# Kernel tuning notes

Hardware: AMD Instinct MI355X
Metric: run time of the kernel (lower is better)

The kernel has to match this reference:

```python
import jax, jax.numpy as jnp
import numpy as np

N = 50000
EH = 500000
ES = 250000
D_IN = 128
D_HID = 128
N_CLS = 47


def _mean_agg(feat, src, dst, n):
    # gather src features, scatter-mean onto dst (DGL copy_u + mean)
    msg = feat[src]                                   # [E, d]
    s = jax.ops.segment_sum(msg, dst, num_segments=n)  # [N, d]
    cnt = jax.ops.segment_sum(jnp.ones((src.shape[0],), feat.dtype), dst, num_segments=n)
    return s / jnp.maximum(cnt, 1.0)[:, None]


def _sage_cv_layer(H, HBar, W, b, hs, hd, ss, sd):
    hbar_new = _mean_agg(HBar, hs, hd, N)             # history etype
    hdelta_new = _mean_agg(H - HBar, ss, sd, N)       # sampled etype
    h_neigh = hbar_new + hdelta_new
    z = jnp.concatenate([H, h_neigh], axis=1)         # [N, 2*d_in]
    return jax.nn.relu(z @ W.T + b)


def setup_inputs() -> dict:
    key = jax.random.key(0)
    ks = jax.random.split(key, 16)
    gain = float(np.sqrt(2.0))  # calculate_gain('relu')

    def xavier(k, shape):
        fan_out, fan_in = shape
        a = gain * np.sqrt(6.0 / (fan_in + fan_out))
        return jax.random.uniform(k, shape, jnp.float32, -a, a)

    return {
        "x": jax.random.normal(ks[0], (N, D_IN), jnp.float32),
        "hbar0": jax.random.normal(ks[1], (N, D_IN), jnp.float32),
        "hbar1": jax.random.normal(ks[2], (N, D_HID), jnp.float32),
        "W0": xavier(ks[3], (D_HID, 2 * D_IN)),
        "b0": jnp.zeros((D_HID,), jnp.float32),
        "W1": xavier(ks[4], (N_CLS, 2 * D_HID)),
        "b1": jnp.zeros((N_CLS,), jnp.float32),
        "hist_src0": jax.random.randint(ks[5], (EH,), 0, N),
        "hist_dst0": jax.random.randint(ks[6], (EH,), 0, N),
        "samp_src0": jax.random.randint(ks[7], (ES,), 0, N),
        "samp_dst0": jax.random.randint(ks[8], (ES,), 0, N),
        "hist_src1": jax.random.randint(ks[9], (EH,), 0, N),
        "hist_dst1": jax.random.randint(ks[10], (EH,), 0, N),
        "samp_src1": jax.random.randint(ks[11], (ES,), 0, N),
        "samp_dst1": jax.random.randint(ks[12], (ES,), 0, N),
    }


def reference(x, hbar0, hbar1, W0, b0, W1, b1,
              hist_src0, hist_dst0, samp_src0, samp_dst0,
              hist_src1, hist_dst1, samp_src1, samp_dst1):
    h = _sage_cv_layer(x, hbar0, W0, b0, hist_src0, hist_dst0, samp_src0, samp_dst0)
    h = _sage_cv_layer(h, hbar1, W1, b1, hist_src1, hist_dst1, samp_src1, samp_dst1)
    return h  # [N, n_classes]
```

## Files before the change

kernel.cpp:

```cpp
#include <hip/hip_runtime.h>

#define D_FEAT 128
#define K_DIM  256
#define EPB 4096

typedef __attribute__((ext_vector_type(8))) short bf16x8;
typedef __attribute__((ext_vector_type(4))) float f32x4;

__device__ __forceinline__ unsigned short f2b(float f) {
    union { float f; unsigned u; } cv; cv.f = f;
    return (unsigned short)((cv.u + 0x7fffu + ((cv.u >> 16) & 1u)) >> 16);
}

__device__ __forceinline__ void addu4(float* a, uint4 v) {
    union { unsigned u; float f; } c;
    c.u = v.x << 16;         a[0] += c.f;
    c.u = v.x & 0xffff0000u; a[1] += c.f;
    c.u = v.y << 16;         a[2] += c.f;
    c.u = v.y & 0xffff0000u; a[3] += c.f;
    c.u = v.z << 16;         a[4] += c.f;
    c.u = v.z & 0xffff0000u; a[5] += c.f;
    c.u = v.w << 16;         a[6] += c.f;
    c.u = v.w & 0xffff0000u; a[7] += c.f;
}

__device__ __forceinline__ long yoff(int y, int EH, int ES) {
    return (long)((y + 1) >> 1) * EH + (long)(y >> 1) * ES;
}


__global__ __launch_bounds__(256)
void histB(const int* __restrict__ hd0, const int* __restrict__ sd0,
           const int* __restrict__ hd1, const int* __restrict__ sd1,
           int EH, int ES, int* __restrict__ bucketCnt, int nb2) {
    int y = blockIdx.y;
    const int* d = (y == 0) ? hd0 : (y == 1) ? sd0 : (y == 2) ? hd1 : sd1;
    int E = (y & 1) ? ES : EH;
    __shared__ int cnt[256];
    int t = threadIdx.x;
    cnt[t] = 0;
    __syncthreads();
    int i0 = blockIdx.x * EPB;
    #pragma unroll
    for (int j = 0; j < 16; ++j) {
        int i = i0 + j * 256 + t;
        if (i < E) atomicAdd(&cnt[d[i] >> 8], 1);
    }
    __syncthreads();
    if (t < nb2 && cnt[t] > 0) atomicAdd(&bucketCnt[y * nb2 + t], cnt[t]);
}

__global__ __launch_bounds__(64)
void scanBuckets(const int* __restrict__ bucketCnt, int* __restrict__ rpBucket,
                 int* __restrict__ bcur, int nb2) {
    int t = threadIdx.x;
    if (t < 4) {
        int run = 0;
        for (int i = 0; i < nb2; ++i) {
            rpBucket[t * (nb2 + 1) + i] = run;
            bcur[t * nb2 + i] = run;
            run += bucketCnt[t * nb2 + i];
        }
        rpBucket[t * (nb2 + 1) + nb2] = run;
    }
}

__global__ __launch_bounds__(256)
void binA(const int* __restrict__ hs0, const int* __restrict__ hd0,
          const int* __restrict__ ss0, const int* __restrict__ sd0,
          const int* __restrict__ hs1, const int* __restrict__ hd1,
          const int* __restrict__ ss1, const int* __restrict__ sd1,
          int EH, int ES, int* __restrict__ bcur, unsigned* __restrict__ recs,
          int nb2) {
    int y = blockIdx.y;
    const int* src = (y == 0) ? hs0 : (y == 1) ? ss0 : (y == 2) ? hs1 : ss1;
    const int* dst = (y == 0) ? hd0 : (y == 1) ? sd0 : (y == 2) ? hd1 : sd1;
    int E = (y & 1) ? ES : EH;
    unsigned* rb = recs + yoff(y, EH, ES);

    __shared__ int cnt[256];
    int t = threadIdx.x;
    cnt[t] = 0;
    __syncthreads();
    int i0 = blockIdx.x * EPB;
    #pragma unroll
    for (int j = 0; j < 16; ++j) {
        int i = i0 + j * 256 + t;
        if (i < E) atomicAdd(&cnt[dst[i] >> 8], 1);
    }
    __syncthreads();
    int c = cnt[t];
    __syncthreads();
    if (t < nb2 && c > 0) cnt[t] = atomicAdd(&bcur[y * nb2 + t], c);
    __syncthreads();
    #pragma unroll
    for (int j = 0; j < 16; ++j) {
        int i = i0 + j * 256 + t;
        if (i < E) {
            int dd = dst[i];
            int slot = atomicAdd(&cnt[dd >> 8], 1);
            rb[slot] = (unsigned)src[i] | ((unsigned)(dd & 255) << 24);
        }
    }
}

__global__ __launch_bounds__(256)
void placeB(const unsigned* __restrict__ recs, const int* __restrict__ rpBucket,
            int* __restrict__ rpAll, int* __restrict__ srcAll,
            int EH, int ES, int n, int nb2) {
    int y = blockIdx.y;
    int b = blockIdx.x;
    int E = (y & 1) ? ES : EH;
    int* rp = rpAll + (size_t)y * (n + 1);
    long off = yoff(y, EH, ES);
    const unsigned* rb = recs + off;
    int* sb = srcAll + off;
    int e0 = rpBucket[y * (nb2 + 1) + b];
    int e1 = rpBucket[y * (nb2 + 1) + b + 1];
    int nodeBase = b << 8;

    __shared__ int cnt[256];
    __shared__ int sh[256];
    int t = threadIdx.x;
    cnt[t] = 0;
    __syncthreads();
    for (int e = e0 + t; e < e1; e += 256)
        atomicAdd(&cnt[rb[e] >> 24], 1);
    __syncthreads();
    sh[t] = cnt[t];
    __syncthreads();
    for (int o = 1; o < 256; o <<= 1) {
        int x = (t >= o) ? sh[t - o] : 0;
        __syncthreads();
        sh[t] += x;
        __syncthreads();
    }
    int base = e0 + (t ? sh[t - 1] : 0);
    if (nodeBase + t < n) rp[nodeBase + t] = base;
    if (b == 0 && t == 0) rp[n] = E;
    cnt[t] = base;
    __syncthreads();
    for (int e = e0 + t; e < e1; e += 256) {
        unsigned r = rb[e];
        int p = atomicAdd(&cnt[r >> 24], 1);
        sb[p] = (int)(r & 0x00FFFFFFu);
    }
}

__global__ __launch_bounds__(256)
void prep_tables(const float4* __restrict__ H, const float4* __restrict__ HBar,
                 ushort4* __restrict__ hb, ushort4* __restrict__ db, int nvec) {
    int i = blockIdx.x * 256 + threadIdx.x;
    if (i >= nvec) return;
    float4 h = H[i], b = HBar[i];
    hb[i] = make_ushort4(f2b(b.x), f2b(b.y), f2b(b.z), f2b(b.w));
    db[i] = make_ushort4(f2b(h.x - b.x), f2b(h.y - b.y), f2b(h.z - b.z), f2b(h.w - b.w));
}

__global__ __launch_bounds__(256)
void conv_weights(const float* __restrict__ W0, unsigned short* __restrict__ Wb0,
                  const float* __restrict__ W1, unsigned short* __restrict__ Wb1) {
    int i = blockIdx.x * 256 + threadIdx.x;
    if (i < 128 * 256) Wb0[i] = f2b(W0[i]);
    if (i < 64 * 256) {
        int r = i >> 8;
        Wb1[i] = (r < 47) ? f2b(W1[i]) : (unsigned short)0;
    }
}

__global__ __launch_bounds__(256)
void aggregate_z(const float* __restrict__ H, const uint4* __restrict__ HB,
                 const uint4* __restrict__ DB,
                 const int* __restrict__ rpH, const int* __restrict__ srcH,
                 const int* __restrict__ rpS, const int* __restrict__ srcS,
                 uint4* __restrict__ z, int n) {
    int g    = blockIdx.x * 16 + (threadIdx.x >> 4);
    int lane = threadIdx.x & 15;
    if (g >= n) return;

    int hb_ = rpH[g], he = rpH[g + 1];
    int sb  = rpS[g], se = rpS[g + 1];

    float a[8] = {0, 0, 0, 0, 0, 0, 0, 0};
    int e = hb_;
    for (; e + 4 <= he; e += 4) {
        int s0 = srcH[e], s1 = srcH[e + 1], s2 = srcH[e + 2], s3 = srcH[e + 3];
        uint4 v0 = HB[(size_t)s0 * 16 + lane];
        uint4 v1 = HB[(size_t)s1 * 16 + lane];
        uint4 v2 = HB[(size_t)s2 * 16 + lane];
        uint4 v3 = HB[(size_t)s3 * 16 + lane];
        addu4(a, v0); addu4(a, v1); addu4(a, v2); addu4(a, v3);
    }
    for (; e < he; ++e) addu4(a, HB[(size_t)srcH[e] * 16 + lane]);

    float d[8] = {0, 0, 0, 0, 0, 0, 0, 0};
    e = sb;
    for (; e + 4 <= se; e += 4) {
        int s0 = srcS[e], s1 = srcS[e + 1], s2 = srcS[e + 2], s3 = srcS[e + 3];
        uint4 v0 = DB[(size_t)s0 * 16 + lane];
        uint4 v1 = DB[(size_t)s1 * 16 + lane];
        uint4 v2 = DB[(size_t)s2 * 16 + lane];
        uint4 v3 = DB[(size_t)s3 * 16 + lane];
        addu4(d, v0); addu4(d, v1); addu4(d, v2); addu4(d, v3);
    }
    for (; e < se; ++e) addu4(d, DB[(size_t)srcS[e] * 16 + lane]);

    float rH = 1.0f / fmaxf((float)(he - hb_), 1.0f);
    float rS = 1.0f / fmaxf((float)(se - sb), 1.0f);

    float nb0 = a[0] * rH + d[0] * rS, nb1 = a[1] * rH + d[1] * rS;
    float nb2 = a[2] * rH + d[2] * rS, nb3 = a[3] * rH + d[3] * rS;
    float nb4 = a[4] * rH + d[4] * rS, nb5 = a[5] * rH + d[5] * rS;
    float nb6 = a[6] * rH + d[6] * rS, nb7 = a[7] * rH + d[7] * rS;
    uint4 rv;
    rv.x = (unsigned)f2b(nb0) | ((unsigned)f2b(nb1) << 16);
    rv.y = (unsigned)f2b(nb2) | ((unsigned)f2b(nb3) << 16);
    rv.z = (unsigned)f2b(nb4) | ((unsigned)f2b(nb5) << 16);
    rv.w = (unsigned)f2b(nb6) | ((unsigned)f2b(nb7) << 16);
    z[(size_t)g * 32 + 16 + lane] = rv;

    const float4* H4 = (const float4*)H;
    float4 l0 = H4[(size_t)g * 32 + lane * 2];
    float4 l1 = H4[(size_t)g * 32 + lane * 2 + 1];
    uint4 lv;
    lv.x = (unsigned)f2b(l0.x) | ((unsigned)f2b(l0.y) << 16);
    lv.y = (unsigned)f2b(l0.z) | ((unsigned)f2b(l0.w) << 16);
    lv.z = (unsigned)f2b(l1.x) | ((unsigned)f2b(l1.y) << 16);
    lv.w = (unsigned)f2b(l1.z) | ((unsigned)f2b(l1.w) << 16);
    z[(size_t)g * 32 + lane] = lv;
}

template<int NT>
__global__ __launch_bounds__(256)
void gemm_mfma(const unsigned short* __restrict__ Z, const unsigned short* __restrict__ Wb,
               const float* __restrict__ bias, float* __restrict__ out, int n, int COLS) {
    int wave = threadIdx.x >> 6;
    int lane = threadIdx.x & 63;
    int m0 = blockIdx.x * 64 + wave * 16;
    int mr = m0 + (lane & 15);
    int mc = (mr < n) ? mr : (n - 1);
    int kq = lane >> 4;

    f32x4 acc[NT] = {};
    const short* Zs = (const short*)Z;
    const short* Ws = (const short*)Wb;

    #pragma unroll
    for (int k0 = 0; k0 < 8; ++k0) {
        int ko = k0 * 32 + kq * 8;
        bf16x8 aF = *(const bf16x8*)(Zs + (size_t)mc * 256 + ko);
        #pragma unroll
        for (int t = 0; t < NT; ++t) {
            bf16x8 bF = *(const bf16x8*)(Ws + (size_t)(t * 16 + (lane & 15)) * 256 + ko);
            acc[t] = __builtin_amdgcn_mfma_f32_16x16x32_bf16(aF, bF, acc[t], 0, 0, 0);
        }
    }

    int cl = lane & 15;
    int rg = (lane >> 4) * 4;
    #pragma unroll
    for (int t = 0; t < NT; ++t) {
        int c = t * 16 + cl;
        if (c >= COLS) continue;
        float bv = bias[c];
        #pragma unroll
        for (int r = 0; r < 4; ++r) {
            int m = m0 + rg + r;
            if (m < n) out[(size_t)m * COLS + c] = fmaxf(acc[t][r] + bv, 0.f);
        }
    }
}

extern "C" void kernel_launch(void* const* d_in, const int* in_sizes, int n_in,
                              void* d_out, int out_size, void* d_ws, size_t ws_size,
                              hipStream_t stream) {
    const float* x     = (const float*)d_in[0];
    const float* hbar0 = (const float*)d_in[1];
    const float* hbar1 = (const float*)d_in[2];
    const float* W0    = (const float*)d_in[3];
    const float* b0    = (const float*)d_in[4];
    const float* W1    = (const float*)d_in[5];
    const float* b1    = (const float*)d_in[6];
    const int* hs0 = (const int*)d_in[7];
    const int* hd0 = (const int*)d_in[8];
    const int* ss0 = (const int*)d_in[9];
    const int* sd0 = (const int*)d_in[10];
    const int* hs1 = (const int*)d_in[11];
    const int* hd1 = (const int*)d_in[12];
    const int* ss1 = (const int*)d_in[13];
    const int* sd1 = (const int*)d_in[14];

    const int n   = in_sizes[0] / D_FEAT;
    const int EH  = in_sizes[7];
    const int ES  = in_sizes[9];
    const int nb2 = (n + 255) / 256;

    int* bucketCnt = (int*)d_ws;
    int* rpBucket  = bucketCnt + 4 * nb2;
    int* bcur      = rpBucket + 4 * (nb2 + 1);
    int* rpAll     = bcur + 4 * nb2;
    int* srcAll    = rpAll + 4 * (size_t)(n + 1);
    size_t int_words = (size_t)12 * nb2 + 4 + 4 * (size_t)(n + 1)
                     + 2 * (size_t)EH + 2 * (size_t)ES;
    int_words = (int_words + 3) & ~(size_t)3;
    float* h1 = (float*)d_ws + int_words;
    unsigned short* hb  = (unsigned short*)(h1 + (size_t)n * D_FEAT);
    unsigned short* db  = hb + (size_t)n * D_FEAT;
    unsigned short* z   = db + (size_t)n * D_FEAT;
    unsigned short* Wb0 = z + (size_t)n * K_DIM;
    unsigned short* Wb1 = Wb0 + 128 * 256;
    unsigned* recs = (unsigned*)z;

    const int* rpH0 = rpAll;
    const int* rpS0 = rpAll + (size_t)(n + 1);
    const int* rpH1 = rpAll + 2 * (size_t)(n + 1);
    const int* rpS1 = rpAll + 3 * (size_t)(n + 1);
    int* srcH0 = srcAll;
    int* srcS0 = srcAll + (size_t)EH;
    int* srcH1 = srcAll + (size_t)EH + ES;
    int* srcS1 = srcAll + 2 * (size_t)EH + ES;

    dim3 blk(256);
    int binb  = (EH + EPB - 1) / EPB;
    int prepb = ((n * 32) + 255) / 256;
    int aggb  = (n + 15) / 16;
    int gemmb = (n + 63) / 64;

    hipMemsetAsync(bucketCnt, 0, 4 * (size_t)nb2 * sizeof(int), stream);
    conv_weights<<<128, blk, 0, stream>>>(W0, Wb0, W1, Wb1);
    histB<<<dim3(binb, 4), blk, 0, stream>>>(hd0, sd0, hd1, sd1, EH, ES, bucketCnt, nb2);
    scanBuckets<<<1, 64, 0, stream>>>(bucketCnt, rpBucket, bcur, nb2);
    binA<<<dim3(binb, 4), blk, 0, stream>>>(hs0, hd0, ss0, sd0, hs1, hd1, ss1, sd1,
                                            EH, ES, bcur, recs, nb2);
    placeB<<<dim3(nb2, 4), blk, 0, stream>>>(recs, rpBucket, rpAll, srcAll, EH, ES, n, nb2);

    prep_tables<<<prepb, blk, 0, stream>>>((const float4*)x, (const float4*)hbar0,
                                           (ushort4*)hb, (ushort4*)db, n * 32);
    aggregate_z<<<aggb, blk, 0, stream>>>(x, (const uint4*)hb, (const uint4*)db,
                                          rpH0, srcH0, rpS0, srcS0, (uint4*)z, n);
    gemm_mfma<8><<<gemmb, blk, 0, stream>>>(z, Wb0, b0, h1, n, 128);

    prep_tables<<<prepb, blk, 0, stream>>>((const float4*)h1, (const float4*)hbar1,
                                           (ushort4*)hb, (ushort4*)db, n * 32);
    aggregate_z<<<aggb, blk, 0, stream>>>(h1, (const uint4*)hb, (const uint4*)db,
                                          rpH1, srcH1, rpS1, srcS1, (uint4*)z, n);
    gemm_mfma<3><<<gemmb, blk, 0, stream>>>(z, Wb1, b1, (float*)d_out, n, 47);
}
```

Measured before the change: 353.2 us.

## Fuse layer-1 table prep into layer-0 GEMM epilogue and widen aggregation

Builds the bf16 tables for both layers in one static prep kernel: hbar0, x−hbar0, hbar1 and the self half of z from x. The layer-0 GEMM epilogue now writes relu output directly as bf16 into z's self half and as (h−hbar1) into the layer-1 delta table. This removes the fp32 h1 buffer, the second prep pass and the self-feature conversion in aggregation. Aggregation now uses a full 64-lane wave per node with eight edges in flight, followed by a shuffle reduction. The cost is more scattered 2-byte stores in the GEMM epilogue, an in-place read/write of z, and a larger workspace because the edge records move out of z.

```diff
diff --git a/kernel.cpp b/kernel.cpp
--- a/kernel.cpp
+++ b/kernel.cpp
@@ -10,6 +10,14 @@
 __device__ __forceinline__ unsigned short f2b(float f) {
     union { float f; unsigned u; } cv; cv.f = f;
     return (unsigned short)((cv.u + 0x7fffu + ((cv.u >> 16) & 1u)) >> 16);
+}
+
+__device__ __forceinline__ unsigned pack2(float lo, float hi) {
+    return (unsigned)f2b(lo) | ((unsigned)f2b(hi) << 16);
+}
+
+__device__ __forceinline__ uint4 pack8(float4 a, float4 b) {
+    return make_uint4(pack2(a.x, a.y), pack2(a.z, a.w), pack2(b.x, b.y), pack2(b.z, b.w));
 }
 
 __device__ __forceinline__ void addu4(float* a, uint4 v) {
@@ -148,13 +156,21 @@
 }
 
 __global__ __launch_bounds__(256)
-void prep_tables(const float4* __restrict__ H, const float4* __restrict__ HBar,
-                 ushort4* __restrict__ hb, ushort4* __restrict__ db, int nvec) {
+void prep_static(const float4* __restrict__ x, const float4* __restrict__ hbar0,
+                 const float4* __restrict__ hbar1,
+                 uint4* __restrict__ hb0, uint4* __restrict__ db0,
+                 uint4* __restrict__ hb1, uint4* __restrict__ z, int n16) {
     int i = blockIdx.x * 256 + threadIdx.x;
-    if (i >= nvec) return;
-    float4 h = H[i], b = HBar[i];
-    hb[i] = make_ushort4(f2b(b.x), f2b(b.y), f2b(b.z), f2b(b.w));
-    db[i] = make_ushort4(f2b(h.x - b.x), f2b(h.y - b.y), f2b(h.z - b.z), f2b(h.w - b.w));
+    if (i >= n16) return;
+    float4 xa = x[i * 2],     xb = x[i * 2 + 1];
+    float4 ba = hbar0[i * 2], bb = hbar0[i * 2 + 1];
+    float4 ca = hbar1[i * 2], cb = hbar1[i * 2 + 1];
+    hb0[i] = pack8(ba, bb);
+    db0[i] = pack8(make_float4(xa.x - ba.x, xa.y - ba.y, xa.z - ba.z, xa.w - ba.w),
+                   make_float4(xb.x - bb.x, xb.y - bb.y, xb.z - bb.z, xb.w - bb.w));
+    hb1[i] = pack8(ca, cb);
+    int g = i >> 4, seg = i & 15;
+    z[(size_t)g * 32 + seg] = pack8(xa, xb);
 }
 
 __global__ __launch_bounds__(256)
@@ -169,65 +185,93 @@
 }
 
 __global__ __launch_bounds__(256)
-void aggregate_z(const float* __restrict__ H, const uint4* __restrict__ HB,
-                 const uint4* __restrict__ DB,
+void aggregate_z(const uint4* __restrict__ HB, const uint4* __restrict__ DB,
                  const int* __restrict__ rpH, const int* __restrict__ srcH,
                  const int* __restrict__ rpS, const int* __restrict__ srcS,
                  uint4* __restrict__ z, int n) {
-    int g    = blockIdx.x * 16 + (threadIdx.x >> 4);
-    int lane = threadIdx.x & 15;
+    int g = blockIdx.x * 4 + (threadIdx.x >> 6);
     if (g >= n) return;
+    int lane = threadIdx.x & 63;
+    int j = lane >> 4, l = lane & 15;
 
     int hb_ = rpH[g], he = rpH[g + 1];
     int sb  = rpS[g], se = rpS[g + 1];
 
     float a[8] = {0, 0, 0, 0, 0, 0, 0, 0};
-    int e = hb_;
-    for (; e + 4 <= he; e += 4) {
-        int s0 = srcH[e], s1 = srcH[e + 1], s2 = srcH[e + 2], s3 = srcH[e + 3];
-        uint4 v0 = HB[(size_t)s0 * 16 + lane];
-        uint4 v1 = HB[(size_t)s1 * 16 + lane];
-        uint4 v2 = HB[(size_t)s2 * 16 + lane];
-        uint4 v3 = HB[(size_t)s3 * 16 + lane];
-        addu4(a, v0); addu4(a, v1); addu4(a, v2); addu4(a, v3);
-    }
-    for (; e < he; ++e) addu4(a, HB[(size_t)srcH[e] * 16 + lane]);
-
+    for (int e0 = hb_; e0 < he; e0 += 8) {
+        int e1 = e0 + j, e2 = e0 + 4 + j;
+        uint4 v1 = make_uint4(0, 0, 0, 0), v2 = make_uint4(0, 0, 0, 0);
+        if (e1 < he) v1 = HB[(size_t)srcH[e1] * 16 + l];
+        if (e2 < he) v2 = HB[(size_t)srcH[e2] * 16 + l];
+        addu4(a, v1); addu4(a, v2);
+    }
     float d[8] = {0, 0, 0, 0, 0, 0, 0, 0};
-    e = sb;
-    for (; e + 4 <= se; e += 4) {
-        int s0 = srcS[e], s1 = srcS[e + 1], s2 = srcS[e + 2], s3 = srcS[e + 3];
-        uint4 v0 = DB[(size_t)s0 * 16 + lane];
-        uint4 v1 = DB[(size_t)s1 * 16 + lane];
-        uint4 v2 = DB[(size_t)s2 * 16 + lane];
-        uint4 v3 = DB[(size_t)s3 * 16 + lane];
-        addu4(d, v0); addu4(d, v1); addu4(d, v2); addu4(d, v3);
-    }
-    for (; e < se; ++e) addu4(d, DB[(size_t)srcS[e] * 16 + lane]);
+    for (int e0 = sb; e0 < se; e0 += 8) {
+        int e1 = e0 + j, e2 = e0 + 4 + j;
+        uint4 v1 = make_uint4(0, 0, 0, 0), v2 = make_uint4(0, 0, 0, 0);
+        if (e1 < se) v1 = DB[(size_t)srcS[e1] * 16 + l];
+        if (e2 < se) v2 = DB[(size_t)srcS[e2] * 16 + l];
+        addu4(d, v1); addu4(d, v2);
+    }
 
     float rH = 1.0f / fmaxf((float)(he - hb_), 1.0f);
     float rS = 1.0f / fmaxf((float)(se - sb), 1.0f);
-
-    float nb0 = a[0] * rH + d[0] * rS, nb1 = a[1] * rH + d[1] * rS;
-    float nb2 = a[2] * rH + d[2] * rS, nb3 = a[3] * rH + d[3] * rS;
-    float nb4 = a[4] * rH + d[4] * rS, nb5 = a[5] * rH + d[5] * rS;
-    float nb6 = a[6] * rH + d[6] * rS, nb7 = a[7] * rH + d[7] * rS;
-    uint4 rv;
-    rv.x = (unsigned)f2b(nb0) | ((unsigned)f2b(nb1) << 16);
-    rv.y = (unsigned)f2b(nb2) | ((unsigned)f2b(nb3) << 16);
-    rv.z = (unsigned)f2b(nb4) | ((unsigned)f2b(nb5) << 16);
-    rv.w = (unsigned)f2b(nb6) | ((unsigned)f2b(nb7) << 16);
-    z[(size_t)g * 32 + 16 + lane] = rv;
-
-    const float4* H4 = (const float4*)H;
-    float4 l0 = H4[(size_t)g * 32 + lane * 2];
-    float4 l1 = H4[(size_t)g * 32 + lane * 2 + 1];
-    uint4 lv;
-    lv.x = (unsigned)f2b(l0.x) | ((unsigned)f2b(l0.y) << 16);
-    lv.y = (unsigned)f2b(l0.z) | ((unsigned)f2b(l0.w) << 16);
-    lv.z = (unsigned)f2b(l1.x) | ((unsigned)f2b(l1.y) << 16);
-    lv.w = (unsigned)f2b(l1.z) | ((unsigned)f2b(l1.w) << 16);
-    z[(size_t)g * 32 + lane] = lv;
+    float s[8];
+    #pragma unroll
+    for (int i = 0; i < 8; ++i) {
+        float v = a[i] * rH + d[i] * rS;
+        v += __shfl_xor(v, 16);
+        v += __shfl_xor(v, 32);
+        s[i] = v;
+    }
+    if (j == 0) {
+        uint4 rv = make_uint4(pack2(s[0], s[1]), pack2(s[2], s[3]),
+                              pack2(s[4], s[5]), pack2(s[6], s[7]));
+        z[(size_t)g * 32 + 16 + l] = rv;
+    }
+}
+
+__global__ __launch_bounds__(256)
+void gemm_mfma_l0(const unsigned short* __restrict__ Z, const unsigned short* __restrict__ Wb,
+                  const float* __restrict__ bias, const float* __restrict__ hbar1,
+                  unsigned short* __restrict__ db1, unsigned short* __restrict__ zl, int n) {
+    int wave = threadIdx.x >> 6;
+    int lane = threadIdx.x & 63;
+    int m0 = blockIdx.x * 64 + wave * 16;
+    int mr = m0 + (lane & 15);
+    int mc = (mr < n) ? mr : (n - 1);
+    int kq = lane >> 4;
+
+    f32x4 acc[8] = {};
+    const short* Zs = (const short*)Z;
+    const short* Ws = (const short*)Wb;
+
+    #pragma unroll
+    for (int k0 = 0; k0 < 8; ++k0) {
+        int ko = k0 * 32 + kq * 8;
+        bf16x8 aF = *(const bf16x8*)(Zs + (size_t)mc * 256 + ko);
+        #pragma unroll
+        for (int t = 0; t < 8; ++t) {
+            bf16x8 bF = *(const bf16x8*)(Ws + (size_t)(t * 16 + (lane & 15)) * 256 + ko);
+            acc[t] = __builtin_amdgcn_mfma_f32_16x16x32_bf16(aF, bF, acc[t], 0, 0, 0);
+        }
+    }
+
+    int cl = lane & 15;
+    int rg = (lane >> 4) * 4;
+    #pragma unroll
+    for (int r = 0; r < 4; ++r) {
+        int m = m0 + rg + r;
+        if (m >= n) continue;
+        #pragma unroll
+        for (int t = 0; t < 8; ++t) {
+            int c = t * 16 + cl;
+            float h = fmaxf(acc[t][r] + bias[c], 0.0f);
+            float hbv = hbar1[(size_t)m * 128 + c];
+            db1[(size_t)m * 128 + c] = f2b(h - hbv);
+            zl[(size_t)m * 256 + c]  = f2b(h);
+        }
+    }
 }
 
 template<int NT>
@@ -300,16 +344,17 @@
     int* bcur      = rpBucket + 4 * (nb2 + 1);
     int* rpAll     = bcur + 4 * nb2;
     int* srcAll    = rpAll + 4 * (size_t)(n + 1);
+    unsigned* recs = (unsigned*)(srcAll + 2 * (size_t)EH + 2 * (size_t)ES);
     size_t int_words = (size_t)12 * nb2 + 4 + 4 * (size_t)(n + 1)
-                     + 2 * (size_t)EH + 2 * (size_t)ES;
+                     + 4 * (size_t)EH + 4 * (size_t)ES;
     int_words = (int_words + 3) & ~(size_t)3;
-    float* h1 = (float*)d_ws + int_words;
-    unsigned short* hb  = (unsigned short*)(h1 + (size_t)n * D_FEAT);
-    unsigned short* db  = hb + (size_t)n * D_FEAT;
-    unsigned short* z   = db + (size_t)n * D_FEAT;
+    unsigned short* hb0 = (unsigned short*)((int*)d_ws + int_words);
+    unsigned short* db0 = hb0 + (size_t)n * D_FEAT;
+    unsigned short* hb1 = db0 + (size_t)n * D_FEAT;
+    unsigned short* db1 = hb1 + (size_t)n * D_FEAT;
+    unsigned short* z   = db1 + (size_t)n * D_FEAT;
     unsigned short* Wb0 = z + (size_t)n * K_DIM;
     unsigned short* Wb1 = Wb0 + 128 * 256;
-    unsigned* recs = (unsigned*)z;
 
     const int* rpH0 = rpAll;
     const int* rpS0 = rpAll + (size_t)(n + 1);
@@ -322,8 +367,8 @@
 
     dim3 blk(256);
     int binb  = (EH + EPB - 1) / EPB;
-    int prepb = ((n * 32) + 255) / 256;
-    int aggb  = (n + 15) / 16;
+    int prepb = ((n * 16) + 255) / 256;
+    int aggb  = (n + 3) / 4;
     int gemmb = (n + 63) / 64;
 
     hipMemsetAsync(bucketCnt, 0, 4 * (size_t)nb2 * sizeof(int), stream);
@@ -333,16 +378,15 @@
     binA<<<dim3(binb, 4), blk, 0, stream>>>(hs0, hd0, ss0, sd0, hs1, hd1, ss1, sd1,
                                             EH, ES, bcur, recs, nb2);
     placeB<<<dim3(nb2, 4), blk, 0, stream>>>(recs, rpBucket, rpAll, srcAll, EH, ES, n, nb2);
-
-    prep_tables<<<prepb, blk, 0, stream>>>((const float4*)x, (const float4*)hbar0,
-                                           (ushort4*)hb, (ushort4*)db, n * 32);
-    aggregate_z<<<aggb, blk, 0, stream>>>(x, (const uint4*)hb, (const uint4*)db,
+    prep_static<<<prepb, blk, 0, stream>>>((const float4*)x, (const float4*)hbar0,
+                                           (const float4*)hbar1, (uint4*)hb0, (uint4*)db0,
+                                           (uint4*)hb1, (uint4*)z, n * 16);
+
+    aggregate_z<<<aggb, blk, 0, stream>>>((const uint4*)hb0, (const uint4*)db0,
                                           rpH0, srcH0, rpS0, srcS0, (uint4*)z, n);
-    gemm_mfma<8><<<gemmb, blk, 0, stream>>>(z, Wb0, b0, h1, n, 128);
-
-    prep_tables<<<prepb, blk, 0, stream>>>((const float4*)h1, (const float4*)hbar1,
-                                           (ushort4*)hb, (ushort4*)db, n * 32);
-    aggregate_z<<<aggb, blk, 0, stream>>>(h1, (const uint4*)hb, (const uint4*)db,
+    gemm_mfma_l0<<<gemmb, blk, 0, stream>>>(z, Wb0, b0, hbar1, db1, z, n);
+
+    aggregate_z<<<aggb, blk, 0, stream>>>((const uint4*)hb1, (const uint4*)db1,
                                           rpH1, srcH1, rpS1, srcS1, (uint4*)z, n);
     gemm_mfma<3><<<gemmb, blk, 0, stream>>>(z, Wb1, b1, (float*)d_out, n, 47);
 }
```

Measured after the change: 351.2 us. Within noise of the previous version (-0.5%).
